# Kernel optimization log

Measured on AMD Instinct MI355X. Metric: run time of the kernel, lower is better.

Reference implementation:

```python
import jax, jax.numpy as jnp
import numpy as np
from jax import lax

THR = 1.0            # spike_threshold
GRAD_WIDTH = 0.5     # sinabs SingleExponential grad_width
GRAD_SCALE = 1.0     # sinabs SingleExponential grad_scale
ABS_WIDTH = THR * GRAD_WIDTH

# SingleSpike with SingleExponential surrogate gradient (Shrestha & Orchard 2018)
@jax.custom_vjp
def spike(v):
    return (v >= THR).astype(v.dtype)

def _spike_fwd(v):
    return (v >= THR).astype(v.dtype), v

def _spike_bwd(v, g):
    sg = (GRAD_SCALE / ABS_WIDTH) * jnp.exp(-jnp.abs(v - THR) / ABS_WIDTH)
    return (g * sg,)

spike.defvjp(_spike_fwd, _spike_bwd)

def avgpool4(x):  # AvgPool2d(4) on NCHW
    n, c, h, w = x.shape
    return x.reshape(n, c, h // 4, 4, w // 4, 4).mean(axis=(3, 5))

def conv7(x, w):  # Conv2d k=7 pad=3 no bias, NCHW/OIHW
    return lax.conv_general_dilated(x, w, (1, 1), [(3, 3), (3, 3)],
                                    dimension_numbers=('NCHW', 'OIHW', 'NCHW'))

def iaf(x):
    """IAF with MembraneSubtract reset. x: (n, t, c, h, w) -> spikes, same shape."""
    xt = jnp.moveaxis(x, 1, 0)  # (t, n, c, h, w)
    def step(v, xin):
        v = v + xin
        s = spike(v)
        return v - s * THR, s
    _, s = lax.scan(step, jnp.zeros_like(xt[0]), xt)
    return jnp.moveaxis(s, 0, 1)

def setup_inputs() -> dict:
    key = jax.random.key(0)
    k0, k1, k2, k3 = jax.random.split(key, 4)
    inp = jax.random.uniform(k0, (8, 2, 256, 256, 64), dtype=jnp.float32)
    w0 = jax.random.normal(k1, (4, 2, 7, 7), jnp.float32) / np.float32(np.sqrt(2 * 49))
    w1 = jax.random.normal(k2, (8, 4, 7, 7), jnp.float32) / np.float32(np.sqrt(4 * 49))
    wl = jax.random.normal(k3, (2, 128), jnp.float32) / np.float32(np.sqrt(128))
    return {"inp": inp, "w0": w0, "w1": w1, "wl": wl}

def reference(inp, w0, w1, wl):
    n, c, y, x, t = inp.shape
    # movedim(-1, 1) then flatten(0, 1): (n, t, c, y, x) -> (n*t, c, y, x)
    data = jnp.moveaxis(inp, -1, 1).reshape(n * t, c, y, x)
    h0 = conv7(avgpool4(data), w0)                          # (n*t, 4, 64, 64)
    s0 = iaf(h0.reshape(n, t, 4, 64, 64)).reshape(n * t, 4, 64, 64)
    h1 = conv7(avgpool4(s0), w1)                            # (n*t, 8, 16, 16)
    s1 = iaf(h1.reshape(n, t, 8, 16, 16)).reshape(n * t, 8, 16, 16)
    feat = avgpool4(s1).reshape(n * t, -1)                  # (n*t, 128)
    out = feat @ wl.T                                       # (n*t, 2)
    return jnp.moveaxis(out.reshape(n, t, 2), 1, -1)        # (n, 2, t)
```

## Files before the change

### kernel.cpp

```cpp
#include <hip/hip_runtime.h>


#define OFF_P0   0
#define OFF_H0   4194304
#define OFF_P1   12582912
#define OFF_H1   13107200

__global__ void pool0_kernel(const float* __restrict__ inp,
                             float* __restrict__ out) {
    int tid = blockIdx.x * blockDim.x + threadIdx.x;
    int t4 = tid & 15;
    int px = (tid >> 4) & 63;
    int py = (tid >> 10) & 63;
    int nc = tid >> 16;
    const float* base = inp + (size_t)nc * 4194304 + (size_t)t4 * 4;
    int y0 = py * 4, x0 = px * 4;
    double a0 = 0, a1 = 0, a2 = 0, a3 = 0;
    #pragma unroll
    for (int dy = 0; dy < 4; ++dy) {
        const float* row = base + ((size_t)(y0 + dy) * 256 + x0) * 64;
        #pragma unroll
        for (int dx = 0; dx < 4; ++dx) {
            const float4 v = *(const float4*)(row + dx * 64);
            a0 += (double)v.x; a1 += (double)v.y;
            a2 += (double)v.z; a3 += (double)v.w;
        }
    }
    float4 o = make_float4((float)(a0 * 0.0625), (float)(a1 * 0.0625),
                           (float)(a2 * 0.0625), (float)(a3 * 0.0625));
    ((float4*)out)[tid] = o;
}

__global__ void conv0_kernel(const float* __restrict__ pooled0,
                             const float* __restrict__ w0,
                             float* __restrict__ h0) {
    __shared__ double w[392];
    for (int i = threadIdx.x; i < 392; i += blockDim.x) w[i] = (double)w0[i];
    __syncthreads();

    int tid = blockIdx.x * blockDim.x + threadIdx.x;
    int t4  = tid & 15;
    int px  = (tid >> 4) & 63;
    int pyp = (tid >> 10) & 31;
    int n   = tid >> 15;
    int py0 = pyp * 2;

    double acc[4][2][4] = {};
    for (int ic = 0; ic < 2; ++ic) {
        const float* in_c = pooled0 + (size_t)(n * 2 + ic) * 262144 + t4 * 4;
        const double* wic = w + ic * 49;
        #pragma unroll
        for (int r = 0; r < 8; ++r) {
            int iy = py0 - 3 + r;
            if (iy < 0 || iy >= 64) continue;
            const float* in_row = in_c + (size_t)iy * 4096;
            #pragma unroll
            for (int kx = 0; kx < 7; ++kx) {
                int ix = px + kx - 3;
                if (ix < 0 || ix >= 64) continue;
                float4 v = *(const float4*)(in_row + ix * 64);
                if (r <= 6) {
                    #pragma unroll
                    for (int oc = 0; oc < 4; ++oc) {
                        double wd = wic[oc * 98 + r * 7 + kx];
                        acc[oc][0][0] += (double)v.x * wd;
                        acc[oc][0][1] += (double)v.y * wd;
                        acc[oc][0][2] += (double)v.z * wd;
                        acc[oc][0][3] += (double)v.w * wd;
                    }
                }
                if (r >= 1) {
                    #pragma unroll
                    for (int oc = 0; oc < 4; ++oc) {
                        double wd = wic[oc * 98 + (r - 1) * 7 + kx];
                        acc[oc][1][0] += (double)v.x * wd;
                        acc[oc][1][1] += (double)v.y * wd;
                        acc[oc][1][2] += (double)v.z * wd;
                        acc[oc][1][3] += (double)v.w * wd;
                    }
                }
            }
        }
    }
    #pragma unroll
    for (int p = 0; p < 2; ++p) {
        size_t ob = (size_t)n * 1048576 + (size_t)(py0 + p) * 4096
                  + (size_t)px * 64 + t4 * 4;
        #pragma unroll
        for (int oc = 0; oc < 4; ++oc) {
            float4 o = make_float4((float)acc[oc][p][0], (float)acc[oc][p][1],
                                   (float)acc[oc][p][2], (float)acc[oc][p][3]);
            *(float4*)(h0 + ob + (size_t)oc * 262144) = o;
        }
    }
}

__global__ __launch_bounds__(64) void iaf0_pool1_kernel(
        const float* __restrict__ h0, float* __restrict__ pooled1) {
    int b   = blockIdx.x;
    int c   = b & 3;
    int pyo = (b >> 2) & 15;
    int n   = b >> 6;
    int lane = threadIdx.x;
    int pxo = lane & 15;
    int dy  = lane >> 4;
    int py  = pyo * 4 + dy;

    const float* base = h0 + (((size_t)(n * 4 + c) * 64 + py) * 64 + pxo * 4) * 64;
    const float4* p0 = (const float4*)(base);
    const float4* p1 = (const float4*)(base + 64);
    const float4* p2 = (const float4*)(base + 128);
    const float4* p3 = (const float4*)(base + 192);

    float v0 = 0.f, v1 = 0.f, v2 = 0.f, v3 = 0.f;
    float sg[64];
    #pragma unroll
    for (int i = 0; i < 16; ++i) {
        float4 x0 = p0[i], x1 = p1[i], x2 = p2[i], x3 = p3[i];
        #define STEP(j, e)                                                    \
        {   float s0_, s1_, s2_, s3_;                                         \
            v0 += x0.e; s0_ = (v0 >= 1.f) ? 1.f : 0.f; v0 -= s0_;             \
            v1 += x1.e; s1_ = (v1 >= 1.f) ? 1.f : 0.f; v1 -= s1_;             \
            v2 += x2.e; s2_ = (v2 >= 1.f) ? 1.f : 0.f; v2 -= s2_;             \
            v3 += x3.e; s3_ = (v3 >= 1.f) ? 1.f : 0.f; v3 -= s3_;             \
            sg[i * 4 + j] = (s0_ + s1_) + (s2_ + s3_);  }
        STEP(0, x) STEP(1, y) STEP(2, z) STEP(3, w)
        #undef STEP
    }
    #pragma unroll
    for (int j = 0; j < 64; ++j) {
        sg[j] += __shfl_xor(sg[j], 16);
        sg[j] += __shfl_xor(sg[j], 32);
    }
    float* outrow = pooled1 + (((size_t)(n * 4 + c) * 16 + pyo) * 16 + pxo) * 64;
    #pragma unroll
    for (int jj = 0; jj < 4; ++jj) {
        int t0 = dy * 4 + jj * 16;
        float4 o = make_float4(sg[t0] * 0.0625f, sg[t0 + 1] * 0.0625f,
                               sg[t0 + 2] * 0.0625f, sg[t0 + 3] * 0.0625f);
        *(float4*)(outrow + t0) = o;
    }
}

__global__ void conv1_kernel(const float* __restrict__ pooled1,
                             const float* __restrict__ w1,
                             float* __restrict__ h1) {
    __shared__ double w[1568];
    for (int i = threadIdx.x; i < 1568; i += blockDim.x) w[i] = (double)w1[i];
    __syncthreads();

    int tid = blockIdx.x * blockDim.x + threadIdx.x;
    int t  = tid & 63;
    int px = (tid >> 6) & 15;
    int py = (tid >> 10) & 15;
    int n  = tid >> 14;
    double acc[8];
    #pragma unroll
    for (int oc = 0; oc < 8; ++oc) acc[oc] = 0.0;

    for (int ic = 0; ic < 4; ++ic) {
        const float* in_c = pooled1 + (size_t)(n * 4 + ic) * 16384;
        const double* wic = w + ic * 49;
        #pragma unroll
        for (int ky = 0; ky < 7; ++ky) {
            int iy = py + ky - 3;
            if (iy < 0 || iy >= 16) continue;
            const float* in_row = in_c + (size_t)iy * 1024 + t;
            const double* wrow = wic + ky * 7;
            #pragma unroll
            for (int kx = 0; kx < 7; ++kx) {
                int ix = px + kx - 3;
                if (ix < 0 || ix >= 16) continue;
                double v = (double)in_row[ix * 64];
                #pragma unroll
                for (int oc = 0; oc < 8; ++oc)
                    acc[oc] += v * wrow[kx + oc * 196];
            }
        }
    }
    size_t ob = (size_t)n * 131072 + (size_t)py * 1024 + px * 64 + t;
    #pragma unroll
    for (int oc = 0; oc < 8; ++oc)
        h1[ob + (size_t)oc * 16384] = (float)acc[oc];
}

__global__ void iaf_kernel(float* __restrict__ buf) {
    int tid = blockIdx.x * blockDim.x + threadIdx.x;
    float4* p = (float4*)(buf + (size_t)tid * 64);
    float v = 0.0f;
    #pragma unroll
    for (int i = 0; i < 16; ++i) {
        float4 x = p[i];
        v += x.x; { float s = (v >= 1.0f) ? 1.0f : 0.0f; v -= s; x.x = s; }
        v += x.y; { float s = (v >= 1.0f) ? 1.0f : 0.0f; v -= s; x.y = s; }
        v += x.z; { float s = (v >= 1.0f) ? 1.0f : 0.0f; v -= s; x.z = s; }
        v += x.w; { float s = (v >= 1.0f) ? 1.0f : 0.0f; v -= s; x.w = s; }
        p[i] = x;
    }
}

__global__ void final_kernel(const float* __restrict__ s1,
                             const float* __restrict__ wl,
                             float* __restrict__ out) {
    int tid = blockIdx.x * blockDim.x + threadIdx.x;
    int t = tid & 63;
    int j = (tid >> 6) & 1;
    int n = tid >> 7;
    double acc = 0.0;
    for (int c = 0; c < 8; ++c) {
        const float* base = s1 + (size_t)(n * 8 + c) * 16384;
        #pragma unroll
        for (int py = 0; py < 4; ++py) {
            #pragma unroll
            for (int px = 0; px < 4; ++px) {
                float ssum = 0.0f;
                #pragma unroll
                for (int dy = 0; dy < 4; ++dy) {
                    const float* row = base + ((size_t)(py * 4 + dy) * 16 + px * 4) * 64 + t;
                    #pragma unroll
                    for (int dx = 0; dx < 4; ++dx)
                        ssum += row[dx * 64];
                }
                float feat = ssum * 0.0625f;
                acc += (double)wl[j * 128 + c * 16 + py * 4 + px] * (double)feat;
            }
        }
    }
    out[(size_t)(n * 2 + j) * 64 + t] = (float)acc;
}

extern "C" void kernel_launch(void* const* d_in, const int* in_sizes, int n_in,
                              void* d_out, int out_size, void* d_ws, size_t ws_size,
                              hipStream_t stream) {
    const float* inp = (const float*)d_in[0];
    const float* w0  = (const float*)d_in[1];
    const float* w1  = (const float*)d_in[2];
    const float* wl  = (const float*)d_in[3];
    float* out = (float*)d_out;
    float* ws  = (float*)d_ws;

    float* pooled0 = ws + OFF_P0;
    float* h0      = ws + OFF_H0;
    float* pooled1 = ws + OFF_P1;
    float* h1      = ws + OFF_H1;

    pool0_kernel<<<4096, 256, 0, stream>>>(inp, pooled0);
    conv0_kernel<<<1024, 256, 0, stream>>>(pooled0, w0, h0);
    iaf0_pool1_kernel<<<512, 64, 0, stream>>>(h0, pooled1);
    conv1_kernel<<<512, 256, 0, stream>>>(pooled1, w1, h1);
    iaf_kernel<<<64, 256, 0, stream>>>(h1);
    final_kernel<<<4, 256, 0, stream>>>(h1, wl, out);
}
```

Measured before the change: 525.6 us.

## Parallelize IAF per pixel with packed spike counts and fuse second pool

Reworks iaf0_pool1 so each thread runs the IAF scan for a single pixel instead of four, giving 256-thread blocks with four times as many threads and far fewer live registers. Spikes are packed as byte counts into 32-bit words and summed over the 4x4 pool window with shuffles. The second IAF is fused with the final average pool and writes a compact feature buffer, and a lighter linear kernel with more blocks reads it, so the final kernel no longer rereads all of h1 serially. Packing four 8-bit counts per word relies on pool sums staying at or below 16.

```diff
diff --git a/kernel.cpp b/kernel.cpp
--- a/kernel.cpp
+++ b/kernel.cpp
@@ -5,6 +5,7 @@
 #define OFF_H0   4194304
 #define OFF_P1   12582912
 #define OFF_H1   13107200
+#define OFF_FT   14155776
 
 __global__ void pool0_kernel(const float* __restrict__ inp,
                              float* __restrict__ out) {
@@ -95,51 +96,52 @@
     }
 }
 
-__global__ __launch_bounds__(64) void iaf0_pool1_kernel(
+__global__ __launch_bounds__(256) void iaf0_pool1_kernel(
         const float* __restrict__ h0, float* __restrict__ pooled1) {
     int b   = blockIdx.x;
     int c   = b & 3;
     int pyo = (b >> 2) & 15;
     int n   = b >> 6;
-    int lane = threadIdx.x;
-    int pxo = lane & 15;
-    int dy  = lane >> 4;
+    int tid = threadIdx.x;
+    int dx  = tid & 3;
+    int dy  = (tid >> 2) & 3;
+    int pxo = tid >> 4;
     int py  = pyo * 4 + dy;
-
-    const float* base = h0 + (((size_t)(n * 4 + c) * 64 + py) * 64 + pxo * 4) * 64;
-    const float4* p0 = (const float4*)(base);
-    const float4* p1 = (const float4*)(base + 64);
-    const float4* p2 = (const float4*)(base + 128);
-    const float4* p3 = (const float4*)(base + 192);
-
-    float v0 = 0.f, v1 = 0.f, v2 = 0.f, v3 = 0.f;
-    float sg[64];
-    #pragma unroll
-    for (int i = 0; i < 16; ++i) {
-        float4 x0 = p0[i], x1 = p1[i], x2 = p2[i], x3 = p3[i];
+    int px  = pxo * 4 + dx;
+
+    const float4* p = (const float4*)(h0 +
+        (((size_t)(n * 4 + c) * 64 + py) * 64 + px) * 64);
+
+    float v = 0.f;
+    unsigned int sp[16];
+    #pragma unroll
+    for (int i = 0; i < 16; ++i) {
+        float4 x = p[i];
+        unsigned int w = 0;
         #define STEP(j, e)                                                    \
-        {   float s0_, s1_, s2_, s3_;                                         \
-            v0 += x0.e; s0_ = (v0 >= 1.f) ? 1.f : 0.f; v0 -= s0_;             \
-            v1 += x1.e; s1_ = (v1 >= 1.f) ? 1.f : 0.f; v1 -= s1_;             \
-            v2 += x2.e; s2_ = (v2 >= 1.f) ? 1.f : 0.f; v2 -= s2_;             \
-            v3 += x3.e; s3_ = (v3 >= 1.f) ? 1.f : 0.f; v3 -= s3_;             \
-            sg[i * 4 + j] = (s0_ + s1_) + (s2_ + s3_);  }
+        {   v += x.e;                                                         \
+            unsigned int s_ = (v >= 1.f) ? 1u : 0u;                           \
+            v -= (float)s_;                                                   \
+            w += s_ << (8 * j); }
         STEP(0, x) STEP(1, y) STEP(2, z) STEP(3, w)
         #undef STEP
-    }
-    #pragma unroll
-    for (int j = 0; j < 64; ++j) {
-        sg[j] += __shfl_xor(sg[j], 16);
-        sg[j] += __shfl_xor(sg[j], 32);
-    }
-    float* outrow = pooled1 + (((size_t)(n * 4 + c) * 16 + pyo) * 16 + pxo) * 64;
-    #pragma unroll
-    for (int jj = 0; jj < 4; ++jj) {
-        int t0 = dy * 4 + jj * 16;
-        float4 o = make_float4(sg[t0] * 0.0625f, sg[t0 + 1] * 0.0625f,
-                               sg[t0 + 2] * 0.0625f, sg[t0 + 3] * 0.0625f);
-        *(float4*)(outrow + t0) = o;
-    }
+        sp[i] = w;
+    }
+    #pragma unroll
+    for (int i = 0; i < 16; ++i) {
+        sp[i] += __shfl_xor(sp[i], 1);
+        sp[i] += __shfl_xor(sp[i], 2);
+        sp[i] += __shfl_xor(sp[i], 4);
+        sp[i] += __shfl_xor(sp[i], 8);
+    }
+    int i = tid & 15;
+    unsigned int s = sp[i];
+    float4 o = make_float4((float)(s & 255u)         * 0.0625f,
+                           (float)((s >> 8)  & 255u) * 0.0625f,
+                           (float)((s >> 16) & 255u) * 0.0625f,
+                           (float)((s >> 24) & 255u) * 0.0625f);
+    float* outp = pooled1 + (((size_t)(n * 4 + c) * 16 + pyo) * 16 + pxo) * 64 + i * 4;
+    *(float4*)outp = o;
 }
 
 __global__ void conv1_kernel(const float* __restrict__ pooled1,
@@ -184,48 +186,67 @@
         h1[ob + (size_t)oc * 16384] = (float)acc[oc];
 }
 
-__global__ void iaf_kernel(float* __restrict__ buf) {
-    int tid = blockIdx.x * blockDim.x + threadIdx.x;
-    float4* p = (float4*)(buf + (size_t)tid * 64);
-    float v = 0.0f;
+__global__ __launch_bounds__(256) void iaf1_pool2_kernel(
+        const float* __restrict__ h1, float* __restrict__ feat) {
+    int b = blockIdx.x;
+    int c = b & 7;
+    int n = b >> 3;
+    int tid = threadIdx.x;
+    int dx  = tid & 3;
+    int dy  = (tid >> 2) & 3;
+    int q   = tid >> 4;
+    int pyo = q >> 2;
+    int pxo = q & 3;
+    int py  = pyo * 4 + dy;
+    int px  = pxo * 4 + dx;
+
+    const float4* p = (const float4*)(h1 +
+        (((size_t)(n * 8 + c) * 16 + py) * 16 + px) * 64);
+
+    float v = 0.f;
+    unsigned int sp[16];
     #pragma unroll
     for (int i = 0; i < 16; ++i) {
         float4 x = p[i];
-        v += x.x; { float s = (v >= 1.0f) ? 1.0f : 0.0f; v -= s; x.x = s; }
-        v += x.y; { float s = (v >= 1.0f) ? 1.0f : 0.0f; v -= s; x.y = s; }
-        v += x.z; { float s = (v >= 1.0f) ? 1.0f : 0.0f; v -= s; x.z = s; }
-        v += x.w; { float s = (v >= 1.0f) ? 1.0f : 0.0f; v -= s; x.w = s; }
-        p[i] = x;
-    }
-}
-
-__global__ void final_kernel(const float* __restrict__ s1,
-                             const float* __restrict__ wl,
-                             float* __restrict__ out) {
-    int tid = blockIdx.x * blockDim.x + threadIdx.x;
+        unsigned int w = 0;
+        #define STEP(j, e)                                                    \
+        {   v += x.e;                                                         \
+            unsigned int s_ = (v >= 1.f) ? 1u : 0u;                           \
+            v -= (float)s_;                                                   \
+            w += s_ << (8 * j); }
+        STEP(0, x) STEP(1, y) STEP(2, z) STEP(3, w)
+        #undef STEP
+        sp[i] = w;
+    }
+    #pragma unroll
+    for (int i = 0; i < 16; ++i) {
+        sp[i] += __shfl_xor(sp[i], 1);
+        sp[i] += __shfl_xor(sp[i], 2);
+        sp[i] += __shfl_xor(sp[i], 4);
+        sp[i] += __shfl_xor(sp[i], 8);
+    }
+    int i = tid & 15;
+    unsigned int s = sp[i];
+    float4 o = make_float4((float)(s & 255u)         * 0.0625f,
+                           (float)((s >> 8)  & 255u) * 0.0625f,
+                           (float)((s >> 16) & 255u) * 0.0625f,
+                           (float)((s >> 24) & 255u) * 0.0625f);
+    int f = c * 16 + q;
+    *(float4*)(feat + ((size_t)n * 128 + f) * 64 + i * 4) = o;
+}
+
+__global__ __launch_bounds__(64) void linear_kernel(
+        const float* __restrict__ feat, const float* __restrict__ wl,
+        float* __restrict__ out) {
+    int tid = blockIdx.x * 64 + threadIdx.x;
     int t = tid & 63;
     int j = (tid >> 6) & 1;
     int n = tid >> 7;
+    const float* fp = feat + (size_t)n * 128 * 64 + t;
+    const float* wp = wl + j * 128;
     double acc = 0.0;
-    for (int c = 0; c < 8; ++c) {
-        const float* base = s1 + (size_t)(n * 8 + c) * 16384;
-        #pragma unroll
-        for (int py = 0; py < 4; ++py) {
-            #pragma unroll
-            for (int px = 0; px < 4; ++px) {
-                float ssum = 0.0f;
-                #pragma unroll
-                for (int dy = 0; dy < 4; ++dy) {
-                    const float* row = base + ((size_t)(py * 4 + dy) * 16 + px * 4) * 64 + t;
-                    #pragma unroll
-                    for (int dx = 0; dx < 4; ++dx)
-                        ssum += row[dx * 64];
-                }
-                float feat = ssum * 0.0625f;
-                acc += (double)wl[j * 128 + c * 16 + py * 4 + px] * (double)feat;
-            }
-        }
-    }
+    for (int f = 0; f < 128; ++f)
+        acc += (double)wp[f] * (double)fp[(size_t)f * 64];
     out[(size_t)(n * 2 + j) * 64 + t] = (float)acc;
 }
 
@@ -243,11 +264,12 @@
     float* h0      = ws + OFF_H0;
     float* pooled1 = ws + OFF_P1;
     float* h1      = ws + OFF_H1;
+    float* feat    = ws + OFF_FT;
 
     pool0_kernel<<<4096, 256, 0, stream>>>(inp, pooled0);
     conv0_kernel<<<1024, 256, 0, stream>>>(pooled0, w0, h0);
-    iaf0_pool1_kernel<<<512, 64, 0, stream>>>(h0, pooled1);
+    iaf0_pool1_kernel<<<512, 256, 0, stream>>>(h0, pooled1);
     conv1_kernel<<<512, 256, 0, stream>>>(pooled1, w1, h1);
-    iaf_kernel<<<64, 256, 0, stream>>>(h1);
-    final_kernel<<<4, 256, 0, stream>>>(h1, wl, out);
-}
+    iaf1_pool2_kernel<<<64, 256, 0, stream>>>(h1, feat);
+    linear_kernel<<<16, 64, 0, stream>>>(feat, wl, out);
+}
```

Measured after the change: 477.3 us. -9.2%, faster.
